# Optimization experiments

Hardware: AMD Instinct MI355X
Metric: run time of the kernel (lower is better)

Reference implementation:

```python
import jax, jax.numpy as jnp
import numpy as np

N_NODES = 100000
N_EDGES = 3200000
IN_CH, HIDDEN, OUT_CH = 256, 16, 16


def setup_inputs() -> dict:
    key = jax.random.key(0)
    k1, k2, k3, k4, k5, k6 = jax.random.split(key, 6)
    x = jax.random.normal(k1, (N_NODES, IN_CH), dtype=jnp.float32)
    edge_index = jax.random.randint(k2, (2, N_EDGES), 0, N_NODES, dtype=jnp.int64)
    W1 = jax.random.normal(k3, (IN_CH, HIDDEN), dtype=jnp.float32) * (1.0 / np.sqrt(IN_CH))
    b1 = jax.random.normal(k4, (HIDDEN,), dtype=jnp.float32) * 0.01
    W2 = jax.random.normal(k5, (HIDDEN, OUT_CH), dtype=jnp.float32) * (1.0 / np.sqrt(HIDDEN))
    b2 = jax.random.normal(k6, (OUT_CH,), dtype=jnp.float32) * 0.01
    return {"x": x, "edge_index": edge_index, "W1": W1, "b1": b1, "W2": W2, "b2": b2}


def gcn_layer(x, edge_index, W, b):
    # Linear projection: [N, in] @ [in, out] + b
    h = x @ W + b
    source, target = edge_index[0], edge_index[1]
    n = x.shape[0]
    # degree of target nodes (in-degree), symmetric normalization (Kipf & Welling 2017)
    deg = jax.ops.segment_sum(jnp.ones_like(target, dtype=h.dtype), target, num_segments=n)
    deg_inv_sqrt = jnp.where(deg > 0, jax.lax.rsqrt(jnp.maximum(deg, 1.0)), 0.0)
    norm = deg_inv_sqrt[source] * deg_inv_sqrt[target]  # [E]
    # gather-scale-scatter: msg = norm * h[source], aggregated by add at target
    msgs = norm[:, None] * h[source]  # [E, out]
    return jax.ops.segment_sum(msgs, target, num_segments=n)


def reference(x, edge_index, W1, b1, W2, b2):
    h = jax.nn.sigmoid(gcn_layer(x, edge_index, W1, b1))
    return jax.nn.sigmoid(gcn_layer(h, edge_index, W2, b2))
```

## Files before the change

### kernel.cpp

```cpp
#include <hip/hip_runtime.h>
#include <hip/hip_bf16.h>

#define IN_CH 256
#define HID 16
#define BS 256
#define CAP 9216
#define CHUNK 4096
#define PBLK 512
#define EPT (CHUNK/PBLK)
#define SORT_CAP CAP

typedef __attribute__((ext_vector_type(8))) short bf16x8;
typedef __attribute__((ext_vector_type(8))) short short8;
typedef __attribute__((ext_vector_type(4))) float floatx4;

static __device__ __forceinline__ short f2bf(float f) {
    __hip_bfloat16 h = __float2bfloat16(f);
    return *reinterpret_cast<short*>(&h);
}

static __device__ __forceinline__ void acc8(float* a, uint4 v) {
    unsigned w;
    w = v.x;
    a[0] += __uint_as_float(w << 16);
    a[1] += __uint_as_float(w & 0xffff0000u);
    w = v.y;
    a[2] += __uint_as_float(w << 16);
    a[3] += __uint_as_float(w & 0xffff0000u);
    w = v.z;
    a[4] += __uint_as_float(w << 16);
    a[5] += __uint_as_float(w & 0xffff0000u);
    w = v.w;
    a[6] += __uint_as_float(w << 16);
    a[7] += __uint_as_float(w & 0xffff0000u);
}

__global__ void k_init(int* __restrict__ gcursor, int nbuk) {
    int t = threadIdx.x;
    if (t < nbuk) gcursor[t] = t * CAP;
}

__global__ __launch_bounds__(PBLK) void k_part(
        const int* __restrict__ src, const int* __restrict__ tgt,
        int* __restrict__ gcursor, unsigned int* __restrict__ csr, int E, int nbuk) {
    __shared__ int lcount[512];
    __shared__ int gspan[512];
    int t = threadIdx.x;
    int base = blockIdx.x * CHUNK;

    lcount[t] = 0;
    __syncthreads();

    int ebuk[EPT], eofs[EPT];
    unsigned epk[EPT];
#pragma unroll
    for (int k = 0; k < EPT; k++) {
        int e = base + t + k * PBLK;
        if (e < E) {
            int s = src[e], tg = tgt[e];
            ebuk[k] = tg >> 8;
            epk[k] = ((unsigned)s << 8) | (unsigned)(tg & 255);
            eofs[k] = atomicAdd(&lcount[ebuk[k]], 1);
        } else {
            ebuk[k] = -1;
        }
    }
    __syncthreads();
    if (t < nbuk) {
        int c = lcount[t];
        if (c > 0) gspan[t] = atomicAdd(&gcursor[t], c);
    }
    __syncthreads();
#pragma unroll
    for (int k = 0; k < EPT; k++) {
        if (ebuk[k] >= 0) {
            int pos = gspan[ebuk[k]] + eofs[k];
            if (pos < (ebuk[k] + 1) * CAP)
                csr[pos] = epk[k];
        }
    }
}

__global__ __launch_bounds__(512) void k_sort(
        const unsigned int* __restrict__ csr, const int* __restrict__ gcursor,
        int* __restrict__ csr2, int* __restrict__ rowptr,
        int* __restrict__ deg, float* __restrict__ dis, int N) {
    __shared__ int lcnt[256];
    __shared__ int lscan[256];
    __shared__ int ssrc[SORT_CAP];
    int t = threadIdx.x, b = blockIdx.x;
    int start = b * CAP;
    int cnt = min(gcursor[b] - start, CAP);
    int end = start + cnt;

    if (t < 256) lcnt[t] = 0;
    __syncthreads();
    for (int p = start + t; p < end; p += 512) atomicAdd(&lcnt[csr[p] & 255], 1);
    __syncthreads();
    int d = 0;
    if (t < 256) { d = lcnt[t]; lscan[t] = d; }
    __syncthreads();
    for (int off = 1; off < 256; off <<= 1) {
        int a = 0;
        if (t < 256 && t >= off) a = lscan[t - off];
        __syncthreads();
        if (t < 256) lscan[t] += a;
        __syncthreads();
    }
    if (t < 256) {
        int excl = lscan[t] - d;
        int n = b * BS + t;
        if (n < N) {
            rowptr[n] = start + excl;
            deg[n] = d;
            dis[n] = (d > 0) ? rsqrtf((float)d) : 0.0f;
        }
        lcnt[t] = excl;
    }
    __syncthreads();
    for (int p = start + t; p < end; p += 512) {
        unsigned pk = csr[p];
        int pos = atomicAdd(&lcnt[pk & 255], 1);
        ssrc[pos] = (int)(pk >> 8);
    }
    __syncthreads();
    for (int i = t; i < cnt; i += 512) csr2[start + i] = ssrc[i];
}

__global__ void k_gemm1(const float* __restrict__ x,
                        const float* __restrict__ W1,
                        const float* __restrict__ b1,
                        const float* __restrict__ dis,
                        short* __restrict__ h1, int N) {
    int lane = threadIdx.x & 63;
    int wave = threadIdx.x >> 6;
    int tile = blockIdx.x * 4 + wave;
    int nb = tile * 16;
    if (nb >= N) return;

    int mc = lane & 15;
    int q  = lane >> 4;

    bf16x8 bfrag[8];
#pragma unroll
    for (int kb = 0; kb < 8; kb++) {
#pragma unroll
        for (int j = 0; j < 8; j++) {
            bfrag[kb][j] = f2bf(W1[(kb * 32 + q * 8 + j) * HID + mc]);
        }
    }

    const float* xrow = x + (size_t)(nb + mc) * IN_CH;
    floatx4 acc = {0.f, 0.f, 0.f, 0.f};
#pragma unroll
    for (int kb = 0; kb < 8; kb++) {
        const floatx4* p = (const floatx4*)(xrow + kb * 32 + q * 8);
        floatx4 v0 = p[0];
        floatx4 v1 = p[1];
        bf16x8 afrag;
#pragma unroll
        for (int j = 0; j < 4; j++) {
            afrag[j]     = f2bf(v0[j]);
            afrag[j + 4] = f2bf(v1[j]);
        }
        acc = __builtin_amdgcn_mfma_f32_16x16x32_bf16(afrag, bfrag[kb], acc, 0, 0, 0);
    }

    float bias = b1[mc];
#pragma unroll
    for (int r = 0; r < 4; r++) {
        int node = nb + q * 4 + r;
        if (node < N) {
            h1[(size_t)node * HID + mc] = f2bf((acc[r] + bias) * dis[node]);
        }
    }
}

__global__ __launch_bounds__(256) void k_agg_mid(
        const short* __restrict__ h1, const int* __restrict__ csr2,
        const int* __restrict__ rowptr, const int* __restrict__ deg,
        const float* __restrict__ dis,
        const float* __restrict__ W2, const float* __restrict__ b2,
        short* __restrict__ h2, int N) {
    __shared__ float w2s[256];
    __shared__ float b2s[16];
    __shared__ float sv[128][17];
    int t = threadIdx.x;
    w2s[t] = W2[t];
    if (t < 16) b2s[t] = b2[t];
    int nl = t >> 1;
    int cg = t & 1;
    int n = blockIdx.x * 128 + nl;

    float a[8] = {0.f, 0.f, 0.f, 0.f, 0.f, 0.f, 0.f, 0.f};
    float d = 0.f;
    if (n < N) {
        d = dis[n];
        int start = rowptr[n], cnt = deg[n];
        const short* hb = h1 + 8 * cg;
        int i = start, end4 = start + (cnt & ~3);
        for (; i < end4; i += 4) {
            int s0 = csr2[i], s1 = csr2[i + 1], s2 = csr2[i + 2], s3 = csr2[i + 3];
            uint4 v0 = *(const uint4*)(hb + 16 * (size_t)s0);
            uint4 v1 = *(const uint4*)(hb + 16 * (size_t)s1);
            uint4 v2 = *(const uint4*)(hb + 16 * (size_t)s2);
            uint4 v3 = *(const uint4*)(hb + 16 * (size_t)s3);
            acc8(a, v0); acc8(a, v1); acc8(a, v2); acc8(a, v3);
        }
        for (; i < start + cnt; i++) {
            uint4 v = *(const uint4*)(hb + 16 * (size_t)csr2[i]);
            acc8(a, v);
        }
    }
#pragma unroll
    for (int j = 0; j < 8; j++)
        sv[nl][8 * cg + j] = 1.0f / (1.0f + __expf(-d * a[j]));
    __syncthreads();
    if (n < N) {
        float o[8];
#pragma unroll
        for (int j = 0; j < 8; j++) o[j] = b2s[8 * cg + j];
#pragma unroll
        for (int k = 0; k < 16; k++) {
            float s = sv[nl][k];
#pragma unroll
            for (int j = 0; j < 8; j++) o[j] += s * w2s[k * 16 + 8 * cg + j];
        }
        short8 pk;
#pragma unroll
        for (int j = 0; j < 8; j++) pk[j] = f2bf(o[j] * d);
        *(short8*)(h2 + 16 * (size_t)n + 8 * cg) = pk;
    }
}

__global__ __launch_bounds__(256) void k_agg_out(
        const short* __restrict__ h2, const int* __restrict__ csr2,
        const int* __restrict__ rowptr, const int* __restrict__ deg,
        const float* __restrict__ dis, float* __restrict__ out, int N) {
    int t = threadIdx.x;
    int nl = t >> 1;
    int cg = t & 1;
    int n = blockIdx.x * 128 + nl;
    if (n >= N) return;
    float d = dis[n];
    int start = rowptr[n], cnt = deg[n];
    float a[8] = {0.f, 0.f, 0.f, 0.f, 0.f, 0.f, 0.f, 0.f};
    const short* hb = h2 + 8 * cg;
    int i = start, end4 = start + (cnt & ~3);
    for (; i < end4; i += 4) {
        int s0 = csr2[i], s1 = csr2[i + 1], s2 = csr2[i + 2], s3 = csr2[i + 3];
        uint4 v0 = *(const uint4*)(hb + 16 * (size_t)s0);
        uint4 v1 = *(const uint4*)(hb + 16 * (size_t)s1);
        uint4 v2 = *(const uint4*)(hb + 16 * (size_t)s2);
        uint4 v3 = *(const uint4*)(hb + 16 * (size_t)s3);
        acc8(a, v0); acc8(a, v1); acc8(a, v2); acc8(a, v3);
    }
    for (; i < start + cnt; i++) {
        uint4 v = *(const uint4*)(hb + 16 * (size_t)csr2[i]);
        acc8(a, v);
    }
    floatx4 o0, o1;
#pragma unroll
    for (int j = 0; j < 4; j++) {
        o0[j] = 1.0f / (1.0f + __expf(-d * a[j]));
        o1[j] = 1.0f / (1.0f + __expf(-d * a[j + 4]));
    }
    float* op = out + 16 * (size_t)n + 8 * cg;
    *(floatx4*)op = o0;
    *(floatx4*)(op + 4) = o1;
}

extern "C" void kernel_launch(void* const* d_in, const int* in_sizes, int n_in,
                              void* d_out, int out_size, void* d_ws, size_t ws_size,
                              hipStream_t stream) {
    const float* x  = (const float*)d_in[0];
    const int*   ei = (const int*)d_in[1];
    const float* W1 = (const float*)d_in[2];
    const float* b1 = (const float*)d_in[3];
    const float* W2 = (const float*)d_in[4];
    const float* b2 = (const float*)d_in[5];
    float* out = (float*)d_out;

    int N = in_sizes[0] / IN_CH;
    int E = in_sizes[1] / 2;
    const int* src = ei;
    const int* tgt = ei + E;

    int NBUK = (N + BS - 1) / BS;

    char* ws = (char*)d_ws;
    auto align256 = [](size_t v) { return (v + 255) & ~(size_t)255; };
    size_t off = 0;
    int*          gcursor = (int*)(ws + off);          off += align256(512 * sizeof(int));
    unsigned int* csr     = (unsigned int*)(ws + off); off += align256((size_t)NBUK * CAP * sizeof(unsigned int));
    int*          csr2    = (int*)(ws + off);          off += align256((size_t)NBUK * CAP * sizeof(int));
    int*          rowptr  = (int*)(ws + off);          off += align256((size_t)N * sizeof(int));
    int*          deg     = (int*)(ws + off);          off += align256((size_t)N * sizeof(int));
    float*        dis     = (float*)(ws + off);        off += align256((size_t)N * sizeof(float));
    short*        h1      = (short*)(ws + off);        off += align256((size_t)N * HID * sizeof(short));
    short*        h2      = (short*)(ws + off);        off += align256((size_t)N * HID * sizeof(short));

    int grid_part = (E + CHUNK - 1) / CHUNK;
    int grid_g1   = ((N + 15) / 16 + 3) / 4;
    int grid_ag   = (N + 127) / 128;

    k_init   <<<1, 512, 0, stream>>>(gcursor, NBUK);
    k_part   <<<grid_part, PBLK, 0, stream>>>(src, tgt, gcursor, csr, E, NBUK);
    k_sort   <<<NBUK, 512, 0, stream>>>(csr, gcursor, csr2, rowptr, deg, dis, N);
    k_gemm1  <<<grid_g1, 256, 0, stream>>>(x, W1, b1, dis, h1, N);
    k_agg_mid<<<grid_ag, 256, 0, stream>>>(h1, csr2, rowptr, deg, dis, W2, b2, h2, N);
    k_agg_out<<<grid_ag, 256, 0, stream>>>(h2, csr2, rowptr, deg, dis, out, N);
}
```

Measured before the change: 290.8 us.

## Split edge lists across thread pairs, add nontemporal hints, replace init kernel with memset

The aggregation kernels now give each node four threads instead of two. Each pair of threads walks alternating edges and combines partial sums with a lane shuffle, which raises memory-level parallelism for nodes with long edge lists. Nontemporal load and store hints are added to the streaming edge, CSR and x accesses so they pollute the cache less. The cursor init kernel is replaced by a hipMemsetAsync, with bucket offsets made relative. The trade-off is more blocks, shuffle overhead, and half the gathers in flight per thread.

```diff
diff --git a/kernel.cpp b/kernel.cpp
--- a/kernel.cpp
+++ b/kernel.cpp
@@ -11,7 +11,7 @@
 #define SORT_CAP CAP
 
 typedef __attribute__((ext_vector_type(8))) short bf16x8;
-typedef __attribute__((ext_vector_type(8))) short short8;
+typedef __attribute__((ext_vector_type(4))) short short4v;
 typedef __attribute__((ext_vector_type(4))) float floatx4;
 
 static __device__ __forceinline__ short f2bf(float f) {
@@ -35,11 +35,6 @@
     a[7] += __uint_as_float(w & 0xffff0000u);
 }
 
-__global__ void k_init(int* __restrict__ gcursor, int nbuk) {
-    int t = threadIdx.x;
-    if (t < nbuk) gcursor[t] = t * CAP;
-}
-
 __global__ __launch_bounds__(PBLK) void k_part(
         const int* __restrict__ src, const int* __restrict__ tgt,
         int* __restrict__ gcursor, unsigned int* __restrict__ csr, int E, int nbuk) {
@@ -57,7 +52,8 @@
     for (int k = 0; k < EPT; k++) {
         int e = base + t + k * PBLK;
         if (e < E) {
-            int s = src[e], tg = tgt[e];
+            int s = __builtin_nontemporal_load(src + e);
+            int tg = __builtin_nontemporal_load(tgt + e);
             ebuk[k] = tg >> 8;
             epk[k] = ((unsigned)s << 8) | (unsigned)(tg & 255);
             eofs[k] = atomicAdd(&lcount[ebuk[k]], 1);
@@ -75,8 +71,8 @@
     for (int k = 0; k < EPT; k++) {
         if (ebuk[k] >= 0) {
             int pos = gspan[ebuk[k]] + eofs[k];
-            if (pos < (ebuk[k] + 1) * CAP)
-                csr[pos] = epk[k];
+            if (pos < CAP)
+                __builtin_nontemporal_store(epk[k], csr + (size_t)ebuk[k] * CAP + pos);
         }
     }
 }
@@ -90,12 +86,13 @@
     __shared__ int ssrc[SORT_CAP];
     int t = threadIdx.x, b = blockIdx.x;
     int start = b * CAP;
-    int cnt = min(gcursor[b] - start, CAP);
+    int cnt = min(gcursor[b], CAP);
     int end = start + cnt;
 
     if (t < 256) lcnt[t] = 0;
     __syncthreads();
-    for (int p = start + t; p < end; p += 512) atomicAdd(&lcnt[csr[p] & 255], 1);
+    for (int p = start + t; p < end; p += 512)
+        atomicAdd(&lcnt[__builtin_nontemporal_load(csr + p) & 255], 1);
     __syncthreads();
     int d = 0;
     if (t < 256) { d = lcnt[t]; lscan[t] = d; }
@@ -119,12 +116,13 @@
     }
     __syncthreads();
     for (int p = start + t; p < end; p += 512) {
-        unsigned pk = csr[p];
+        unsigned pk = __builtin_nontemporal_load(csr + p);
         int pos = atomicAdd(&lcnt[pk & 255], 1);
         ssrc[pos] = (int)(pk >> 8);
     }
     __syncthreads();
-    for (int i = t; i < cnt; i += 512) csr2[start + i] = ssrc[i];
+    for (int i = t; i < cnt; i += 512)
+        __builtin_nontemporal_store(ssrc[i], csr2 + start + i);
 }
 
 __global__ void k_gemm1(const float* __restrict__ x,
@@ -155,8 +153,8 @@
 #pragma unroll
     for (int kb = 0; kb < 8; kb++) {
         const floatx4* p = (const floatx4*)(xrow + kb * 32 + q * 8);
-        floatx4 v0 = p[0];
-        floatx4 v1 = p[1];
+        floatx4 v0 = __builtin_nontemporal_load(p);
+        floatx4 v1 = __builtin_nontemporal_load(p + 1);
         bf16x8 afrag;
 #pragma unroll
         for (int j = 0; j < 4; j++) {
@@ -184,52 +182,57 @@
         short* __restrict__ h2, int N) {
     __shared__ float w2s[256];
     __shared__ float b2s[16];
-    __shared__ float sv[128][17];
+    __shared__ float sv[64][17];
     int t = threadIdx.x;
     w2s[t] = W2[t];
     if (t < 16) b2s[t] = b2[t];
-    int nl = t >> 1;
-    int cg = t & 1;
-    int n = blockIdx.x * 128 + nl;
+    int nl  = t >> 2;
+    int par = t & 1;
+    int cg  = (t >> 1) & 1;
+    int n = blockIdx.x * 64 + nl;
 
     float a[8] = {0.f, 0.f, 0.f, 0.f, 0.f, 0.f, 0.f, 0.f};
     float d = 0.f;
     if (n < N) {
         d = dis[n];
-        int start = rowptr[n], cnt = deg[n];
+        int start = __builtin_nontemporal_load(rowptr + n);
+        int cnt   = __builtin_nontemporal_load(deg + n);
         const short* hb = h1 + 8 * cg;
-        int i = start, end4 = start + (cnt & ~3);
-        for (; i < end4; i += 4) {
-            int s0 = csr2[i], s1 = csr2[i + 1], s2 = csr2[i + 2], s3 = csr2[i + 3];
+        int i = start + par, end = start + cnt;
+        for (; i + 2 < end; i += 4) {
+            int s0 = __builtin_nontemporal_load(csr2 + i);
+            int s1 = __builtin_nontemporal_load(csr2 + i + 2);
             uint4 v0 = *(const uint4*)(hb + 16 * (size_t)s0);
             uint4 v1 = *(const uint4*)(hb + 16 * (size_t)s1);
-            uint4 v2 = *(const uint4*)(hb + 16 * (size_t)s2);
-            uint4 v3 = *(const uint4*)(hb + 16 * (size_t)s3);
-            acc8(a, v0); acc8(a, v1); acc8(a, v2); acc8(a, v3);
-        }
-        for (; i < start + cnt; i++) {
-            uint4 v = *(const uint4*)(hb + 16 * (size_t)csr2[i]);
-            acc8(a, v);
-        }
-    }
-#pragma unroll
-    for (int j = 0; j < 8; j++)
-        sv[nl][8 * cg + j] = 1.0f / (1.0f + __expf(-d * a[j]));
+            acc8(a, v0); acc8(a, v1);
+        }
+        if (i < end) {
+            int s0 = __builtin_nontemporal_load(csr2 + i);
+            uint4 v0 = *(const uint4*)(hb + 16 * (size_t)s0);
+            acc8(a, v0);
+        }
+    }
+#pragma unroll
+    for (int j = 0; j < 8; j++) a[j] += __shfl_xor(a[j], 1);
+#pragma unroll
+    for (int j = 0; j < 4; j++)
+        sv[nl][8 * cg + 4 * par + j] = 1.0f / (1.0f + __expf(-d * a[4 * par + j]));
     __syncthreads();
     if (n < N) {
-        float o[8];
-#pragma unroll
-        for (int j = 0; j < 8; j++) o[j] = b2s[8 * cg + j];
+        int sub = t & 3;
+        float o[4];
+#pragma unroll
+        for (int j = 0; j < 4; j++) o[j] = b2s[4 * sub + j];
 #pragma unroll
         for (int k = 0; k < 16; k++) {
             float s = sv[nl][k];
 #pragma unroll
-            for (int j = 0; j < 8; j++) o[j] += s * w2s[k * 16 + 8 * cg + j];
-        }
-        short8 pk;
-#pragma unroll
-        for (int j = 0; j < 8; j++) pk[j] = f2bf(o[j] * d);
-        *(short8*)(h2 + 16 * (size_t)n + 8 * cg) = pk;
+            for (int j = 0; j < 4; j++) o[j] += s * w2s[k * 16 + 4 * sub + j];
+        }
+        short4v pk;
+#pragma unroll
+        for (int j = 0; j < 4; j++) pk[j] = f2bf(o[j] * d);
+        *(short4v*)(h2 + 16 * (size_t)n + 4 * sub) = pk;
     }
 }
 
@@ -238,36 +241,36 @@
         const int* __restrict__ rowptr, const int* __restrict__ deg,
         const float* __restrict__ dis, float* __restrict__ out, int N) {
     int t = threadIdx.x;
-    int nl = t >> 1;
-    int cg = t & 1;
-    int n = blockIdx.x * 128 + nl;
+    int nl  = t >> 2;
+    int par = t & 1;
+    int cg  = (t >> 1) & 1;
+    int n = blockIdx.x * 64 + nl;
     if (n >= N) return;
     float d = dis[n];
-    int start = rowptr[n], cnt = deg[n];
+    int start = __builtin_nontemporal_load(rowptr + n);
+    int cnt   = __builtin_nontemporal_load(deg + n);
     float a[8] = {0.f, 0.f, 0.f, 0.f, 0.f, 0.f, 0.f, 0.f};
     const short* hb = h2 + 8 * cg;
-    int i = start, end4 = start + (cnt & ~3);
-    for (; i < end4; i += 4) {
-        int s0 = csr2[i], s1 = csr2[i + 1], s2 = csr2[i + 2], s3 = csr2[i + 3];
+    int i = start + par, end = start + cnt;
+    for (; i + 2 < end; i += 4) {
+        int s0 = __builtin_nontemporal_load(csr2 + i);
+        int s1 = __builtin_nontemporal_load(csr2 + i + 2);
         uint4 v0 = *(const uint4*)(hb + 16 * (size_t)s0);
         uint4 v1 = *(const uint4*)(hb + 16 * (size_t)s1);
-        uint4 v2 = *(const uint4*)(hb + 16 * (size_t)s2);
-        uint4 v3 = *(const uint4*)(hb + 16 * (size_t)s3);
-        acc8(a, v0); acc8(a, v1); acc8(a, v2); acc8(a, v3);
-    }
-    for (; i < start + cnt; i++) {
-        uint4 v = *(const uint4*)(hb + 16 * (size_t)csr2[i]);
-        acc8(a, v);
-    }
-    floatx4 o0, o1;
-#pragma unroll
-    for (int j = 0; j < 4; j++) {
-        o0[j] = 1.0f / (1.0f + __expf(-d * a[j]));
-        o1[j] = 1.0f / (1.0f + __expf(-d * a[j + 4]));
-    }
-    float* op = out + 16 * (size_t)n + 8 * cg;
-    *(floatx4*)op = o0;
-    *(floatx4*)(op + 4) = o1;
+        acc8(a, v0); acc8(a, v1);
+    }
+    if (i < end) {
+        int s0 = __builtin_nontemporal_load(csr2 + i);
+        uint4 v0 = *(const uint4*)(hb + 16 * (size_t)s0);
+        acc8(a, v0);
+    }
+#pragma unroll
+    for (int j = 0; j < 8; j++) a[j] += __shfl_xor(a[j], 1);
+    floatx4 o;
+#pragma unroll
+    for (int j = 0; j < 4; j++)
+        o[j] = 1.0f / (1.0f + __expf(-d * a[4 * par + j]));
+    *(floatx4*)(out + 16 * (size_t)n + 8 * cg + 4 * par) = o;
 }
 
 extern "C" void kernel_launch(void* const* d_in, const int* in_sizes, int n_in,
@@ -302,9 +305,9 @@
 
     int grid_part = (E + CHUNK - 1) / CHUNK;
     int grid_g1   = ((N + 15) / 16 + 3) / 4;
-    int grid_ag   = (N + 127) / 128;
-
-    k_init   <<<1, 512, 0, stream>>>(gcursor, NBUK);
+    int grid_ag   = (N + 63) / 64;
+
+    hipMemsetAsync(gcursor, 0, 512 * sizeof(int), stream);
     k_part   <<<grid_part, PBLK, 0, stream>>>(src, tgt, gcursor, csr, E, NBUK);
     k_sort   <<<NBUK, 512, 0, stream>>>(csr, gcursor, csr2, rowptr, deg, dis, N);
     k_gemm1  <<<grid_g1, 256, 0, stream>>>(x, W1, b1, dis, h1, N);
```

New measurement: 394.0 us. +35.5%, slower.

## Use nontemporal loads, prefetch CSR indices, and replace init kernel with memset

Applied to the files above, without the earlier changes.

Replaces the cursor-init kernel with a memset by making bucket cursors relative offsets rather than absolute positions. Edge and feature reads now use nontemporal loads so streaming data bypasses cache retention. The two aggregation loops software-pipeline the next four neighbor indices while the current gathers are in flight, hiding index-load latency. Together these aim to trim launch overhead and memory latency, at the cost of more registers in the aggregation kernels.

```diff
diff --git a/kernel.cpp b/kernel.cpp
--- a/kernel.cpp
+++ b/kernel.cpp
@@ -35,11 +35,6 @@
     a[7] += __uint_as_float(w & 0xffff0000u);
 }
 
-__global__ void k_init(int* __restrict__ gcursor, int nbuk) {
-    int t = threadIdx.x;
-    if (t < nbuk) gcursor[t] = t * CAP;
-}
-
 __global__ __launch_bounds__(PBLK) void k_part(
         const int* __restrict__ src, const int* __restrict__ tgt,
         int* __restrict__ gcursor, unsigned int* __restrict__ csr, int E, int nbuk) {
@@ -57,7 +52,8 @@
     for (int k = 0; k < EPT; k++) {
         int e = base + t + k * PBLK;
         if (e < E) {
-            int s = src[e], tg = tgt[e];
+            int s  = __builtin_nontemporal_load(src + e);
+            int tg = __builtin_nontemporal_load(tgt + e);
             ebuk[k] = tg >> 8;
             epk[k] = ((unsigned)s << 8) | (unsigned)(tg & 255);
             eofs[k] = atomicAdd(&lcount[ebuk[k]], 1);
@@ -75,8 +71,8 @@
     for (int k = 0; k < EPT; k++) {
         if (ebuk[k] >= 0) {
             int pos = gspan[ebuk[k]] + eofs[k];
-            if (pos < (ebuk[k] + 1) * CAP)
-                csr[pos] = epk[k];
+            if (pos < CAP)
+                csr[(size_t)ebuk[k] * CAP + pos] = epk[k];
         }
     }
 }
@@ -90,7 +86,7 @@
     __shared__ int ssrc[SORT_CAP];
     int t = threadIdx.x, b = blockIdx.x;
     int start = b * CAP;
-    int cnt = min(gcursor[b] - start, CAP);
+    int cnt = min(gcursor[b], CAP);
     int end = start + cnt;
 
     if (t < 256) lcnt[t] = 0;
@@ -155,8 +151,8 @@
 #pragma unroll
     for (int kb = 0; kb < 8; kb++) {
         const floatx4* p = (const floatx4*)(xrow + kb * 32 + q * 8);
-        floatx4 v0 = p[0];
-        floatx4 v1 = p[1];
+        floatx4 v0 = __builtin_nontemporal_load(p);
+        floatx4 v1 = __builtin_nontemporal_load(p + 1);
         bf16x8 afrag;
 #pragma unroll
         for (int j = 0; j < 4; j++) {
@@ -198,16 +194,24 @@
         d = dis[n];
         int start = rowptr[n], cnt = deg[n];
         const short* hb = h1 + 8 * cg;
-        int i = start, end4 = start + (cnt & ~3);
-        for (; i < end4; i += 4) {
+        int i = start, end4 = start + (cnt & ~3), end = start + cnt;
+        if (i < end4) {
             int s0 = csr2[i], s1 = csr2[i + 1], s2 = csr2[i + 2], s3 = csr2[i + 3];
-            uint4 v0 = *(const uint4*)(hb + 16 * (size_t)s0);
-            uint4 v1 = *(const uint4*)(hb + 16 * (size_t)s1);
-            uint4 v2 = *(const uint4*)(hb + 16 * (size_t)s2);
-            uint4 v3 = *(const uint4*)(hb + 16 * (size_t)s3);
-            acc8(a, v0); acc8(a, v1); acc8(a, v2); acc8(a, v3);
-        }
-        for (; i < start + cnt; i++) {
+            for (;;) {
+                uint4 v0 = *(const uint4*)(hb + 16 * (size_t)s0);
+                uint4 v1 = *(const uint4*)(hb + 16 * (size_t)s1);
+                uint4 v2 = *(const uint4*)(hb + 16 * (size_t)s2);
+                uint4 v3 = *(const uint4*)(hb + 16 * (size_t)s3);
+                i += 4;
+                bool more = (i < end4);
+                int n0, n1, n2, n3;
+                if (more) { n0 = csr2[i]; n1 = csr2[i + 1]; n2 = csr2[i + 2]; n3 = csr2[i + 3]; }
+                acc8(a, v0); acc8(a, v1); acc8(a, v2); acc8(a, v3);
+                if (!more) break;
+                s0 = n0; s1 = n1; s2 = n2; s3 = n3;
+            }
+        }
+        for (; i < end; i++) {
             uint4 v = *(const uint4*)(hb + 16 * (size_t)csr2[i]);
             acc8(a, v);
         }
@@ -246,16 +250,24 @@
     int start = rowptr[n], cnt = deg[n];
     float a[8] = {0.f, 0.f, 0.f, 0.f, 0.f, 0.f, 0.f, 0.f};
     const short* hb = h2 + 8 * cg;
-    int i = start, end4 = start + (cnt & ~3);
-    for (; i < end4; i += 4) {
+    int i = start, end4 = start + (cnt & ~3), end = start + cnt;
+    if (i < end4) {
         int s0 = csr2[i], s1 = csr2[i + 1], s2 = csr2[i + 2], s3 = csr2[i + 3];
-        uint4 v0 = *(const uint4*)(hb + 16 * (size_t)s0);
-        uint4 v1 = *(const uint4*)(hb + 16 * (size_t)s1);
-        uint4 v2 = *(const uint4*)(hb + 16 * (size_t)s2);
-        uint4 v3 = *(const uint4*)(hb + 16 * (size_t)s3);
-        acc8(a, v0); acc8(a, v1); acc8(a, v2); acc8(a, v3);
-    }
-    for (; i < start + cnt; i++) {
+        for (;;) {
+            uint4 v0 = *(const uint4*)(hb + 16 * (size_t)s0);
+            uint4 v1 = *(const uint4*)(hb + 16 * (size_t)s1);
+            uint4 v2 = *(const uint4*)(hb + 16 * (size_t)s2);
+            uint4 v3 = *(const uint4*)(hb + 16 * (size_t)s3);
+            i += 4;
+            bool more = (i < end4);
+            int n0, n1, n2, n3;
+            if (more) { n0 = csr2[i]; n1 = csr2[i + 1]; n2 = csr2[i + 2]; n3 = csr2[i + 3]; }
+            acc8(a, v0); acc8(a, v1); acc8(a, v2); acc8(a, v3);
+            if (!more) break;
+            s0 = n0; s1 = n1; s2 = n2; s3 = n3;
+        }
+    }
+    for (; i < end; i++) {
         uint4 v = *(const uint4*)(hb + 16 * (size_t)csr2[i]);
         acc8(a, v);
     }
@@ -304,7 +316,7 @@
     int grid_g1   = ((N + 15) / 16 + 3) / 4;
     int grid_ag   = (N + 127) / 128;
 
-    k_init   <<<1, 512, 0, stream>>>(gcursor, NBUK);
+    hipMemsetAsync(gcursor, 0, 512 * sizeof(int), stream);
     k_part   <<<grid_part, PBLK, 0, stream>>>(src, tgt, gcursor, csr, E, NBUK);
     k_sort   <<<NBUK, 512, 0, stream>>>(csr, gcursor, csr2, rowptr, deg, dis, N);
     k_gemm1  <<<grid_g1, 256, 0, stream>>>(x, W1, b1, dis, h1, N);
```

New measurement: 285.9 us. Within noise of the previous version (-1.7%).
